# Optimization experiments

Hardware: AMD Instinct MI355X
Metric: run time of the kernel (lower is better)

The kernel has to match this reference:

```python
import math
import jax, jax.numpy as jnp
import numpy as np

B, S, D, H, L, V, W, FF = 2, 1024, 512, 8, 6, 32000, 64, 2048
HD = D // H
PAD = 0


def setup_inputs() -> dict:
    key = jax.random.key(0)
    ks = jax.random.split(key, 8)
    init = lambda k, shape: jax.random.normal(k, shape, jnp.float32) * 0.02
    # avoid pad_token_id=0 so no row of the attention mask is fully masked (torch would NaN there too)
    input_ids = jax.random.randint(ks[0], (B, S), 1, V)
    return dict(
        input_ids=input_ids,
        emb=init(ks[1], (V, D)),
        Wqkv=init(ks[2], (L, 3 * D, D)), bqkv=jnp.zeros((L, 3 * D), jnp.float32),
        Wo=init(ks[3], (L, D, D)), bo=jnp.zeros((L, D), jnp.float32),
        W1=init(ks[4], (L, 2 * FF, D)), b1=jnp.zeros((L, 2 * FF), jnp.float32),
        W2=init(ks[5], (L, D, FF)), b2=jnp.zeros((L, D), jnp.float32),
        ln1_g=jnp.ones((L, D), jnp.float32), ln1_b=jnp.zeros((L, D), jnp.float32),
        ln2_g=jnp.ones((L, D), jnp.float32), ln2_b=jnp.zeros((L, D), jnp.float32),
        lnf_g=jnp.ones((D,), jnp.float32), lnf_b=jnp.zeros((D,), jnp.float32),
    )


def _ln(x, g, b, eps=1e-5):
    m = x.mean(-1, keepdims=True)
    v = x.var(-1, keepdims=True)  # biased, matches torch LayerNorm
    return (x - m) / jnp.sqrt(v + eps) * g + b


def _pos_enc(seq_len, d_model):
    pos = jnp.arange(seq_len, dtype=jnp.float32)[:, None]
    div = jnp.exp(jnp.arange(0, d_model, 2, dtype=jnp.float32) * (-math.log(10000.0) / d_model))
    pe = jnp.zeros((seq_len, d_model), jnp.float32)
    pe = pe.at[:, 0::2].set(jnp.sin(pos * div))
    pe = pe.at[:, 1::2].set(jnp.cos(pos * div))
    return pe


def _forward(input_ids, emb, Wqkv, bqkv, Wo, bo, W1, b1, W2, b2,
             ln1_g, ln1_b, ln2_g, ln2_b, lnf_g, lnf_b):
    NEG = jnp.finfo(jnp.float32).min
    idx = jnp.arange(S)
    rel = idx[:, None] - idx[None, :]                      # [S,S], i - j
    win = (jnp.arange(H) + 1) * W                          # per-head window sizes
    valid = (rel[None] >= 0) & (rel[None] < win[:, None, None])  # [H,S,S]
    not_pad = input_ids != PAD                             # [B,S] key padding
    vis = valid[None, :, :, :] & not_pad[:, None, None, :] # [B,H,S,S]
    mask = jnp.where(vis, 0.0, NEG).astype(jnp.float32)

    x = emb[input_ids] + _pos_enc(S, D)                    # [B,S,D]
    for l in range(L):
        # self-attention (torch nn.MultiheadAttention, batch_first)
        qkv = x @ Wqkv[l].T + bqkv[l]                      # [B,S,3D]
        q, k, v = jnp.split(qkv, 3, axis=-1)
        q = q.reshape(B, S, H, HD).transpose(0, 2, 1, 3)
        k = k.reshape(B, S, H, HD).transpose(0, 2, 1, 3)
        v = v.reshape(B, S, H, HD).transpose(0, 2, 1, 3)
        scores = jnp.einsum('bhqd,bhkd->bhqk', q, k) / math.sqrt(HD) + mask
        p = jax.nn.softmax(scores, axis=-1)
        a = jnp.einsum('bhqk,bhkd->bhqd', p, v).transpose(0, 2, 1, 3).reshape(B, S, D)
        a = a @ Wo[l].T + bo[l]
        x = _ln(x + a, ln1_g[l], ln1_b[l])
        # SwiGLU-style FFN: linear1 -> chunk -> a * silu(b) -> linear2
        h = x @ W1[l].T + b1[l]
        u, g = jnp.split(h, 2, axis=-1)
        ff = (u * jax.nn.silu(g)) @ W2[l].T + b2[l]
        x = _ln(x + ff, ln2_g[l], ln2_b[l])
    x = _ln(x, lnf_g, lnf_b)
    return x @ emb.T                                       # tied lm_head, no bias


def reference(input_ids, emb, Wqkv, bqkv, Wo, bo, W1, b1, W2, b2,
              ln1_g, ln1_b, ln2_g, ln2_b, lnf_g, lnf_b):
    return _forward(input_ids, emb, Wqkv, bqkv, Wo, bo, W1, b1, W2, b2,
                    ln1_g, ln1_b, ln2_g, ln2_b, lnf_g, lnf_b)
```

## Files before the change

### kernel.cpp

```cpp
#include <hip/hip_runtime.h>

#define SEQ    1024
#define DIM    512
#define NHEAD  8
#define NLAYER 6
#define FFDIM  2048
#define HDIM   64
#define BATCH  2
#define VOCAB  32000
#define ROWS   (BATCH * SEQ)

typedef __attribute__((ext_vector_type(8))) __bf16 bf16x8;
typedef __attribute__((ext_vector_type(4))) float  f32x4;

__device__ __forceinline__ unsigned short f2bf(float f) {
    unsigned int u = __float_as_uint(f);
    u += 0x7FFFu + ((u >> 16) & 1u);
    return (unsigned short)(u >> 16);
}
__device__ __forceinline__ float bf2f(unsigned short u) {
    return __uint_as_float(((unsigned int)u) << 16);
}
__device__ __forceinline__ float lo_f(unsigned int u) { return __uint_as_float(u << 16); }
__device__ __forceinline__ float hi_f(unsigned int u) { return __uint_as_float(u & 0xFFFF0000u); }
__device__ __forceinline__ unsigned int pack2(float a, float b) {
    return (unsigned int)f2bf(a) | ((unsigned int)f2bf(b) << 16);
}

__global__ __launch_bounds__(256) void cvt_kernel(const float* __restrict__ in,
                                                  unsigned short* __restrict__ out) {
    int base = (blockIdx.x * 256 + threadIdx.x) * 8;
    float4 a = *(const float4*)(in + base);
    float4 b = *(const float4*)(in + base + 4);
    *(uint4*)(out + base) = make_uint4(pack2(a.x, a.y), pack2(a.z, a.w),
                                       pack2(b.x, b.y), pack2(b.z, b.w));
}

__global__ __launch_bounds__(256) void embed_kernel(const int* __restrict__ ids,
                                                    const float* __restrict__ emb,
                                                    unsigned short* __restrict__ x) {
    int t8   = blockIdx.x * 256 + threadIdx.x;
    int base = t8 * 8;
    int row  = base >> 9;
    int d0   = base & (DIM - 1);
    int s    = row & (SEQ - 1);
    int id   = ids[row];
    const float* er = emb + (size_t)id * DIM + d0;
    float4 ea = *(const float4*)(er);
    float4 eb = *(const float4*)(er + 4);
    float e[8] = {ea.x, ea.y, ea.z, ea.w, eb.x, eb.y, eb.z, eb.w};
    unsigned int ou[4];
#pragma unroll
    for (int m = 0; m < 4; ++m) {
        int de = d0 + 2 * m;
        float div = expf((float)de * -0.017988946039015984f);
        float arg = (float)s * div;
        ou[m] = pack2(e[2 * m] + sinf(arg), e[2 * m + 1] + cosf(arg));
    }
    *(uint4*)(x + base) = make_uint4(ou[0], ou[1], ou[2], ou[3]);
}

template <int MODE>
__global__ __launch_bounds__(256) void gemm_kernel(const unsigned short* __restrict__ A,
                                                   const unsigned short* __restrict__ W,
                                                   const float* __restrict__ bias,
                                                   void* __restrict__ Cout,
                                                   int M, int N, int K,
                                                   unsigned short* __restrict__ vT) {
    __shared__ __align__(16) unsigned short As[128 * 72];
    __shared__ __align__(16) unsigned short Bs[128 * 72];
    const int tid  = threadIdx.x;
    const int nwg = (int)(gridDim.x * gridDim.y);
    const int bid = (int)(blockIdx.y * gridDim.x + blockIdx.x);
    const int cpx = nwg >> 3;
    const int wk  = (bid & 7) * cpx + (bid >> 3);
    const int m0  = (wk & 15) * 128;
    const int n0  = (wk >> 4) * 128;
    const int lane = tid & 63;
    const int wv   = tid >> 6;
    const int wr   = wv >> 1, wc = wv & 1;
    const int frow = lane & 15, quad = lane >> 4;

    f32x4 acc[4][4] = {};

    const int sr = tid >> 3;
    const int sc = (tid & 7) * 8;
    const unsigned short* Ag = A + (size_t)(m0 + sr) * K + sc;
    const unsigned short* Wg = W + (size_t)(n0 + sr) * K + sc;

    for (int k0 = 0; k0 < K; k0 += 64) {
#pragma unroll
        for (int p = 0; p < 4; ++p) {
            *(uint4*)&As[(sr + p * 32) * 72 + sc] = *(const uint4*)(Ag + (size_t)(p * 32) * K + k0);
            *(uint4*)&Bs[(sr + p * 32) * 72 + sc] = *(const uint4*)(Wg + (size_t)(p * 32) * K + k0);
        }
        __syncthreads();
#pragma unroll
        for (int kk = 0; kk < 64; kk += 32) {
            bf16x8 af[4], bfr[4];
#pragma unroll
            for (int t = 0; t < 4; ++t) {
                af[t]  = *(const bf16x8*)&As[(wr * 64 + t * 16 + frow) * 72 + kk + quad * 8];
                bfr[t] = *(const bf16x8*)&Bs[(wc * 64 + t * 16 + frow) * 72 + kk + quad * 8];
            }
#pragma unroll
            for (int am = 0; am < 4; ++am)
#pragma unroll
                for (int bn = 0; bn < 4; ++bn)
                    acc[am][bn] = __builtin_amdgcn_mfma_f32_16x16x32_bf16(af[am], bfr[bn], acc[am][bn], 0, 0, 0);
        }
        __syncthreads();
    }

#pragma unroll
    for (int am = 0; am < 4; ++am) {
#pragma unroll
        for (int bn = 0; bn < 4; ++bn) {
            int col  = n0 + wc * 64 + bn * 16 + frow;
            float bv = bias ? bias[col] : 0.0f;
            int rowb = m0 + wr * 64 + am * 16 + quad * 4;
            if (MODE == 2 && col >= 1024) {
                float v0 = acc[am][bn][0] + bv;
                float v1 = acc[am][bn][1] + bv;
                float v2 = acc[am][bn][2] + bv;
                float v3 = acc[am][bn][3] + bv;
                *(uint2*)&vT[(size_t)(col - 1024) * ROWS + rowb] =
                    make_uint2(pack2(v0, v1), pack2(v2, v3));
            } else {
#pragma unroll
                for (int r = 0; r < 4; ++r) {
                    int row = rowb + r;
                    float v = acc[am][bn][r] + bv;
                    if (MODE == 1)      ((float*)Cout)[(size_t)row * N + col] = v;
                    else if (MODE == 2) ((unsigned short*)Cout)[(size_t)row * 1024 + col] = f2bf(v);
                    else                ((unsigned short*)Cout)[(size_t)row * N + col] = f2bf(v);
                }
            }
        }
    }
}

__global__ __launch_bounds__(512) void attn_kernel(const unsigned short* __restrict__ qk,
                                                   const unsigned short* __restrict__ vT,
                                                   unsigned short* __restrict__ out) {
    __shared__ __align__(16) unsigned short P_lds[8][16 * 40];
    const int tid  = threadIdx.x;
    const int w    = tid >> 6, lane = tid & 63;
    const int c    = lane & 15, g = lane >> 4;
    const int b    = blockIdx.x >> 6;
    const int qt   = blockIdx.x & 63;
    const int h    = w;
    const int qbase = qt * 16;
    const int win   = (h + 1) * 64;
    const int qmax  = qbase + 15;
    int kbs = qbase - win + 1; if (kbs < 0) kbs = 0; kbs &= ~31;

    const size_t tok0 = (size_t)b * SEQ;

    const unsigned short* qp = qk + (tok0 + qbase + c) * 1024 + h * HDIM + g * 8;
    const bf16x8 qf0 = *(const bf16x8*)qp;
    const bf16x8 qf1 = *(const bf16x8*)(qp + 32);

    f32x4 o[4] = {};
    float m[4]    = {-3.0e38f, -3.0e38f, -3.0e38f, -3.0e38f};
    float lsum[4] = {};

    unsigned short* pl = P_lds[w];

    for (int kb = kbs; kb <= qmax; kb += 32) {
        f32x4 s[2] = {};
#pragma unroll
        for (int st = 0; st < 2; ++st) {
            const unsigned short* kp = qk + (tok0 + kb + st * 16 + c) * 1024 + DIM + h * HDIM + g * 8;
            bf16x8 kf0 = *(const bf16x8*)kp;
            bf16x8 kf1 = *(const bf16x8*)(kp + 32);
            s[st] = __builtin_amdgcn_mfma_f32_16x16x32_bf16(qf0, kf0, s[st], 0, 0, 0);
            s[st] = __builtin_amdgcn_mfma_f32_16x16x32_bf16(qf1, kf1, s[st], 0, 0, 0);
        }
        float sm[2][4];
        bool  va[2][4];
        float tmax[4];
#pragma unroll
        for (int r = 0; r < 4; ++r) {
            int i  = qbase + 4 * g + r;
            int j0 = kb + c, j1 = j0 + 16;
            bool v0 = (unsigned)(i - j0) < (unsigned)win;
            bool v1 = (unsigned)(i - j1) < (unsigned)win;
            va[0][r] = v0; va[1][r] = v1;
            sm[0][r] = v0 ? s[0][r] * 0.125f : -3.0e38f;
            sm[1][r] = v1 ? s[1][r] * 0.125f : -3.0e38f;
            float t = fmaxf(sm[0][r], sm[1][r]);
#pragma unroll
            for (int off = 1; off < 16; off <<= 1) t = fmaxf(t, __shfl_xor(t, off));
            tmax[r] = t;
        }
#pragma unroll
        for (int r = 0; r < 4; ++r) {
            float mnew = fmaxf(m[r], tmax[r]);
            float scal = __expf(m[r] - mnew);
            float p0 = va[0][r] ? __expf(sm[0][r] - mnew) : 0.0f;
            float p1 = va[1][r] ? __expf(sm[1][r] - mnew) : 0.0f;
            float rs = p0 + p1;
#pragma unroll
            for (int off = 1; off < 16; off <<= 1) rs += __shfl_xor(rs, off);
            lsum[r] = lsum[r] * scal + rs;
            m[r] = mnew;
#pragma unroll
            for (int t = 0; t < 4; ++t) o[t][r] *= scal;
            pl[(4 * g + r) * 40 + c]      = f2bf(p0);
            pl[(4 * g + r) * 40 + c + 16] = f2bf(p1);
        }
        bf16x8 pf = *(const bf16x8*)&pl[c * 40 + g * 8];
#pragma unroll
        for (int t = 0; t < 4; ++t) {
            const unsigned short* vp = vT + (size_t)(h * HDIM + t * 16 + c) * ROWS + tok0 + kb + g * 8;
            bf16x8 vf = *(const bf16x8*)vp;
            o[t] = __builtin_amdgcn_mfma_f32_16x16x32_bf16(pf, vf, o[t], 0, 0, 0);
        }
    }

    float inv[4];
#pragma unroll
    for (int r = 0; r < 4; ++r) inv[r] = 1.0f / lsum[r];
#pragma unroll
    for (int t = 0; t < 4; ++t)
#pragma unroll
        for (int r = 0; r < 4; ++r)
            out[(tok0 + qbase + 4 * g + r) * DIM + h * HDIM + t * 16 + c] = f2bf(o[t][r] * inv[r]);
}

__global__ __launch_bounds__(256) void ln_kernel(const unsigned short* __restrict__ xin,
                                                 const unsigned short* __restrict__ res,
                                                 const float* __restrict__ g,
                                                 const float* __restrict__ bta,
                                                 unsigned short* __restrict__ out) {
    const int tid = threadIdx.x;
    const int w   = tid >> 6, lane = tid & 63;
    const int row = blockIdx.x * 4 + w;
    const int c0  = lane * 8;
    const size_t base = (size_t)row * DIM + c0;

    uint4 xv = *(const uint4*)(xin + base);
    float v[8] = {lo_f(xv.x), hi_f(xv.x), lo_f(xv.y), hi_f(xv.y),
                  lo_f(xv.z), hi_f(xv.z), lo_f(xv.w), hi_f(xv.w)};
    if (res) {
        uint4 rv = *(const uint4*)(res + base);
        v[0] += lo_f(rv.x); v[1] += hi_f(rv.x); v[2] += lo_f(rv.y); v[3] += hi_f(rv.y);
        v[4] += lo_f(rv.z); v[5] += hi_f(rv.z); v[6] += lo_f(rv.w); v[7] += hi_f(rv.w);
    }
    float sum = 0.0f, sq = 0.0f;
#pragma unroll
    for (int t = 0; t < 8; ++t) { sum += v[t]; sq += v[t] * v[t]; }
#pragma unroll
    for (int off = 32; off >= 1; off >>= 1) { sum += __shfl_xor(sum, off); sq += __shfl_xor(sq, off); }
    float mean = sum * (1.0f / DIM);
    float var  = sq * (1.0f / DIM) - mean * mean;
    float rstd = rsqrtf(var + 1e-5f);

    float4 ga = *(const float4*)(g + c0);
    float4 gb = *(const float4*)(g + c0 + 4);
    float4 ba = *(const float4*)(bta + c0);
    float4 bb = *(const float4*)(bta + c0 + 4);
    float gf[8] = {ga.x, ga.y, ga.z, ga.w, gb.x, gb.y, gb.z, gb.w};
    float bf[8] = {ba.x, ba.y, ba.z, ba.w, bb.x, bb.y, bb.z, bb.w};
    unsigned int o[4];
#pragma unroll
    for (int mm = 0; mm < 4; ++mm) {
        float a0 = (v[2 * mm]     - mean) * rstd * gf[2 * mm]     + bf[2 * mm];
        float a1 = (v[2 * mm + 1] - mean) * rstd * gf[2 * mm + 1] + bf[2 * mm + 1];
        o[mm] = pack2(a0, a1);
    }
    *(uint4*)(out + base) = make_uint4(o[0], o[1], o[2], o[3]);
}

__global__ __launch_bounds__(256) void swiglu_kernel(const unsigned short* __restrict__ h,
                                                     unsigned short* __restrict__ o) {
    int t8   = blockIdx.x * 256 + threadIdx.x;
    int base = t8 * 8;
    int r = base >> 11;
    int c = base & (FFDIM - 1);
    const unsigned short* hr = h + (size_t)r * (2 * FFDIM);
    uint4 uv = *(const uint4*)(hr + c);
    uint4 gv = *(const uint4*)(hr + FFDIM + c);
    float u[8] = {lo_f(uv.x), hi_f(uv.x), lo_f(uv.y), hi_f(uv.y),
                  lo_f(uv.z), hi_f(uv.z), lo_f(uv.w), hi_f(uv.w)};
    float gg[8] = {lo_f(gv.x), hi_f(gv.x), lo_f(gv.y), hi_f(gv.y),
                   lo_f(gv.z), hi_f(gv.z), lo_f(gv.w), hi_f(gv.w)};
    unsigned int ov[4];
#pragma unroll
    for (int m = 0; m < 4; ++m) {
        float g0 = gg[2 * m],     s0 = g0 / (1.0f + expf(-g0));
        float g1 = gg[2 * m + 1], s1 = g1 / (1.0f + expf(-g1));
        ov[m] = pack2(u[2 * m] * s0, u[2 * m + 1] * s1);
    }
    *(uint4*)(o + (size_t)r * FFDIM + c) = make_uint4(ov[0], ov[1], ov[2], ov[3]);
}

extern "C" void kernel_launch(void* const* d_in, const int* in_sizes, int n_in,
                              void* d_out, int out_size, void* d_ws, size_t ws_size,
                              hipStream_t stream) {
    const int*   ids  = (const int*)d_in[0];
    const float* emb  = (const float*)d_in[1];
    const float* Wqkv = (const float*)d_in[2];
    const float* bqkv = (const float*)d_in[3];
    const float* Wo   = (const float*)d_in[4];
    const float* bo   = (const float*)d_in[5];
    const float* W1   = (const float*)d_in[6];
    const float* b1   = (const float*)d_in[7];
    const float* W2   = (const float*)d_in[8];
    const float* b2   = (const float*)d_in[9];
    const float* ln1g = (const float*)d_in[10];
    const float* ln1b = (const float*)d_in[11];
    const float* ln2g = (const float*)d_in[12];
    const float* ln2b = (const float*)d_in[13];
    const float* lnfg = (const float*)d_in[14];
    const float* lnfb = (const float*)d_in[15];

    unsigned short* x    = (unsigned short*)d_ws;
    unsigned short* qk   = x    + (size_t)ROWS * DIM;
    unsigned short* vT   = qk   + (size_t)ROWS * 2 * DIM;
    unsigned short* attn = vT   + (size_t)DIM * ROWS;
    unsigned short* proj = attn + (size_t)ROWS * DIM;
    unsigned short* hbuf = proj + (size_t)ROWS * DIM;
    unsigned short* ffin = hbuf + (size_t)ROWS * 2 * FFDIM;
    unsigned short* WqkvB = ffin + (size_t)ROWS * FFDIM;
    unsigned short* WoB   = WqkvB + (size_t)3 * DIM * DIM;
    unsigned short* W1B   = WoB   + (size_t)DIM * DIM;
    unsigned short* W2B   = W1B   + (size_t)2 * FFDIM * DIM;
    unsigned short* embB  = qk;

    embed_kernel<<<ROWS * DIM / (256 * 8), 256, 0, stream>>>(ids, emb, x);

    for (int l = 0; l < NLAYER; ++l) {
        cvt_kernel<<<3 * DIM * DIM / 2048, 256, 0, stream>>>(Wqkv + (size_t)l * 3 * DIM * DIM, WqkvB);
        cvt_kernel<<<DIM * DIM / 2048, 256, 0, stream>>>(Wo + (size_t)l * DIM * DIM, WoB);
        cvt_kernel<<<2 * FFDIM * DIM / 2048, 256, 0, stream>>>(W1 + (size_t)l * 2 * FFDIM * DIM, W1B);
        cvt_kernel<<<DIM * FFDIM / 2048, 256, 0, stream>>>(W2 + (size_t)l * DIM * FFDIM, W2B);

        gemm_kernel<2><<<dim3(16, 12), 256, 0, stream>>>(x, WqkvB, bqkv + l * 3 * DIM,
                                                         qk, ROWS, 3 * DIM, DIM, vT);
        attn_kernel<<<BATCH * (SEQ / 16), 512, 0, stream>>>(qk, vT, attn);
        gemm_kernel<0><<<dim3(16, 4), 256, 0, stream>>>(attn, WoB, bo + l * DIM,
                                                        proj, ROWS, DIM, DIM, nullptr);
        ln_kernel<<<ROWS / 4, 256, 0, stream>>>(x, proj, ln1g + l * DIM, ln1b + l * DIM, x);
        gemm_kernel<0><<<dim3(16, 32), 256, 0, stream>>>(x, W1B, b1 + l * 2 * FFDIM,
                                                         hbuf, ROWS, 2 * FFDIM, DIM, nullptr);
        swiglu_kernel<<<ROWS * FFDIM / (256 * 8), 256, 0, stream>>>(hbuf, ffin);
        gemm_kernel<0><<<dim3(16, 4), 256, 0, stream>>>(ffin, W2B, b2 + l * DIM,
                                                        attn , ROWS, DIM, FFDIM, nullptr);
        ln_kernel<<<ROWS / 4, 256, 0, stream>>>(x, attn, ln2g + l * DIM, ln2b + l * DIM, x);
    }
    ln_kernel<<<ROWS / 4, 256, 0, stream>>>(x, nullptr, lnfg, lnfb, x);
    cvt_kernel<<<VOCAB * DIM / 2048, 256, 0, stream>>>(emb, embB);
    gemm_kernel<1><<<dim3(16, VOCAB / 128), 256, 0, stream>>>(x, embB, nullptr,
                                                              d_out, ROWS, VOCAB, DIM, nullptr);
}
```

Measured before the change: 1.303 ms.

## Load GEMM tiles directly into LDS and convert all weights upfront

The GEMM tile loads now use global_load_lds to write straight into shared memory, which skips the register staging step. The padded 72-element row stride is dropped because the direct loads need a contiguous layout, so fragment reads may hit LDS bank conflicts. All layer weights and the embedding are converted to bf16 once, into dedicated workspace regions, before the layer loop instead of per layer. This cuts the number of small conversion launches at the cost of more workspace.

```diff
diff --git a/kernel.cpp b/kernel.cpp
--- a/kernel.cpp
+++ b/kernel.cpp
@@ -67,8 +67,8 @@
                                                    void* __restrict__ Cout,
                                                    int M, int N, int K,
                                                    unsigned short* __restrict__ vT) {
-    __shared__ __align__(16) unsigned short As[128 * 72];
-    __shared__ __align__(16) unsigned short Bs[128 * 72];
+    __shared__ __align__(16) unsigned short As[128 * 64];
+    __shared__ __align__(16) unsigned short Bs[128 * 64];
     const int tid  = threadIdx.x;
     const int nwg = (int)(gridDim.x * gridDim.y);
     const int bid = (int)(blockIdx.y * gridDim.x + blockIdx.x);
@@ -83,16 +83,22 @@
 
     f32x4 acc[4][4] = {};
 
-    const int sr = tid >> 3;
-    const int sc = (tid & 7) * 8;
-    const unsigned short* Ag = A + (size_t)(m0 + sr) * K + sc;
-    const unsigned short* Wg = W + (size_t)(n0 + sr) * K + sc;
+    const int srow = wv * 32 + (lane >> 3);
+    const int scol = (lane & 7) * 8;
+    const unsigned short* Ag = A + (size_t)(m0 + srow) * K + scol;
+    const unsigned short* Wg = W + (size_t)(n0 + srow) * K + scol;
+    unsigned short* Asw = &As[(wv * 32) * 64];
+    unsigned short* Bsw = &Bs[(wv * 32) * 64];
 
     for (int k0 = 0; k0 < K; k0 += 64) {
 #pragma unroll
         for (int p = 0; p < 4; ++p) {
-            *(uint4*)&As[(sr + p * 32) * 72 + sc] = *(const uint4*)(Ag + (size_t)(p * 32) * K + k0);
-            *(uint4*)&Bs[(sr + p * 32) * 72 + sc] = *(const uint4*)(Wg + (size_t)(p * 32) * K + k0);
+            __builtin_amdgcn_global_load_lds(
+                (const __attribute__((address_space(1))) void*)(Ag + (size_t)(p * 8) * K + k0),
+                (__attribute__((address_space(3))) void*)(Asw + p * 8 * 64), 16, 0, 0);
+            __builtin_amdgcn_global_load_lds(
+                (const __attribute__((address_space(1))) void*)(Wg + (size_t)(p * 8) * K + k0),
+                (__attribute__((address_space(3))) void*)(Bsw + p * 8 * 64), 16, 0, 0);
         }
         __syncthreads();
 #pragma unroll
@@ -100,8 +106,8 @@
             bf16x8 af[4], bfr[4];
 #pragma unroll
             for (int t = 0; t < 4; ++t) {
-                af[t]  = *(const bf16x8*)&As[(wr * 64 + t * 16 + frow) * 72 + kk + quad * 8];
-                bfr[t] = *(const bf16x8*)&Bs[(wc * 64 + t * 16 + frow) * 72 + kk + quad * 8];
+                af[t]  = *(const bf16x8*)&As[(wr * 64 + t * 16 + frow) * 64 + kk + quad * 8];
+                bfr[t] = *(const bf16x8*)&Bs[(wc * 64 + t * 16 + frow) * 64 + kk + quad * 8];
             }
 #pragma unroll
             for (int am = 0; am < 4; ++am)
@@ -324,34 +330,34 @@
     unsigned short* hbuf = proj + (size_t)ROWS * DIM;
     unsigned short* ffin = hbuf + (size_t)ROWS * 2 * FFDIM;
     unsigned short* WqkvB = ffin + (size_t)ROWS * FFDIM;
-    unsigned short* WoB   = WqkvB + (size_t)3 * DIM * DIM;
-    unsigned short* W1B   = WoB   + (size_t)DIM * DIM;
-    unsigned short* W2B   = W1B   + (size_t)2 * FFDIM * DIM;
-    unsigned short* embB  = qk;
+    unsigned short* WoB   = WqkvB + (size_t)NLAYER * 3 * DIM * DIM;
+    unsigned short* W1B   = WoB   + (size_t)NLAYER * DIM * DIM;
+    unsigned short* W2B   = W1B   + (size_t)NLAYER * 2 * FFDIM * DIM;
+    unsigned short* embB  = W2B   + (size_t)NLAYER * DIM * FFDIM;
+
+    cvt_kernel<<<NLAYER * 3 * DIM * DIM / 2048, 256, 0, stream>>>(Wqkv, WqkvB);
+    cvt_kernel<<<NLAYER * DIM * DIM / 2048, 256, 0, stream>>>(Wo, WoB);
+    cvt_kernel<<<NLAYER * 2 * FFDIM * DIM / 2048, 256, 0, stream>>>(W1, W1B);
+    cvt_kernel<<<NLAYER * DIM * FFDIM / 2048, 256, 0, stream>>>(W2, W2B);
+    cvt_kernel<<<VOCAB * DIM / 2048, 256, 0, stream>>>(emb, embB);
 
     embed_kernel<<<ROWS * DIM / (256 * 8), 256, 0, stream>>>(ids, emb, x);
 
     for (int l = 0; l < NLAYER; ++l) {
-        cvt_kernel<<<3 * DIM * DIM / 2048, 256, 0, stream>>>(Wqkv + (size_t)l * 3 * DIM * DIM, WqkvB);
-        cvt_kernel<<<DIM * DIM / 2048, 256, 0, stream>>>(Wo + (size_t)l * DIM * DIM, WoB);
-        cvt_kernel<<<2 * FFDIM * DIM / 2048, 256, 0, stream>>>(W1 + (size_t)l * 2 * FFDIM * DIM, W1B);
-        cvt_kernel<<<DIM * FFDIM / 2048, 256, 0, stream>>>(W2 + (size_t)l * DIM * FFDIM, W2B);
-
-        gemm_kernel<2><<<dim3(16, 12), 256, 0, stream>>>(x, WqkvB, bqkv + l * 3 * DIM,
-                                                         qk, ROWS, 3 * DIM, DIM, vT);
+        gemm_kernel<2><<<dim3(16, 12), 256, 0, stream>>>(x, WqkvB + (size_t)l * 3 * DIM * DIM,
+                                                         bqkv + l * 3 * DIM, qk, ROWS, 3 * DIM, DIM, vT);
         attn_kernel<<<BATCH * (SEQ / 16), 512, 0, stream>>>(qk, vT, attn);
-        gemm_kernel<0><<<dim3(16, 4), 256, 0, stream>>>(attn, WoB, bo + l * DIM,
-                                                        proj, ROWS, DIM, DIM, nullptr);
+        gemm_kernel<0><<<dim3(16, 4), 256, 0, stream>>>(attn, WoB + (size_t)l * DIM * DIM,
+                                                        bo + l * DIM, proj, ROWS, DIM, DIM, nullptr);
         ln_kernel<<<ROWS / 4, 256, 0, stream>>>(x, proj, ln1g + l * DIM, ln1b + l * DIM, x);
-        gemm_kernel<0><<<dim3(16, 32), 256, 0, stream>>>(x, W1B, b1 + l * 2 * FFDIM,
-                                                         hbuf, ROWS, 2 * FFDIM, DIM, nullptr);
+        gemm_kernel<0><<<dim3(16, 32), 256, 0, stream>>>(x, W1B + (size_t)l * 2 * FFDIM * DIM,
+                                                         b1 + l * 2 * FFDIM, hbuf, ROWS, 2 * FFDIM, DIM, nullptr);
         swiglu_kernel<<<ROWS * FFDIM / (256 * 8), 256, 0, stream>>>(hbuf, ffin);
-        gemm_kernel<0><<<dim3(16, 4), 256, 0, stream>>>(ffin, W2B, b2 + l * DIM,
-                                                        attn , ROWS, DIM, FFDIM, nullptr);
+        gemm_kernel<0><<<dim3(16, 4), 256, 0, stream>>>(ffin, W2B + (size_t)l * DIM * FFDIM,
+                                                        b2 + l * DIM, attn , ROWS, DIM, FFDIM, nullptr);
         ln_kernel<<<ROWS / 4, 256, 0, stream>>>(x, attn, ln2g + l * DIM, ln2b + l * DIM, x);
     }
     ln_kernel<<<ROWS / 4, 256, 0, stream>>>(x, nullptr, lnfg, lnfb, x);
-    cvt_kernel<<<VOCAB * DIM / 2048, 256, 0, stream>>>(emb, embB);
     gemm_kernel<1><<<dim3(16, VOCAB / 128), 256, 0, stream>>>(x, embB, nullptr,
                                                               d_out, ROWS, VOCAB, DIM, nullptr);
 }
```

After: 1.352 ms. 3.8% more time.
